# Kernel optimization log

Measured on AMD Instinct MI355X. Metric: run time of the kernel, lower is better.

## Reference

```python
import jax, jax.numpy as jnp
import numpy as np

BLANK = 0
T, N, C, S = 1024, 64, 128, 128


def setup_inputs() -> dict:
    key = jax.random.key(0)
    k1, k2, k3, k4 = jax.random.split(key, 4)
    logits = jax.random.normal(k1, (T, N, C), dtype=jnp.float32)
    log_probs = jax.nn.log_softmax(logits, axis=-1)
    targets = jax.random.randint(k2, (N, S), 1, C).astype(jnp.int64)  # non-blank labels
    input_lengths = jax.random.randint(k3, (N,), T // 2, T + 1).astype(jnp.int32)
    target_lengths = jax.random.randint(k4, (N,), S // 2, S + 1).astype(jnp.int32)
    return {"log_probs": log_probs, "targets": targets,
            "input_lengths": input_lengths, "target_lengths": target_lengths}


def _ctc_loss(log_probs, targets, input_lengths, target_lengths):
    Tt, Nn, Cc = log_probs.shape
    Ss = targets.shape[1]
    Sx = 2 * Ss + 1  # extended target length (blanks interleaved)
    neg_inf = jnp.asarray(-jnp.inf, log_probs.dtype)

    ext = jnp.full((Nn, Sx), BLANK, dtype=jnp.int32).at[:, 1::2].set(targets.astype(jnp.int32))
    # emission log-prob of each extended state at each time: [T, N, Sx]
    emit = jnp.take_along_axis(log_probs, jnp.broadcast_to(ext[None], (Tt, Nn, Sx)), axis=2)
    # skip transition allowed when label[s] != label[s-2] (and s >= 2)
    skip = jnp.concatenate([jnp.zeros((Nn, 2), bool), ext[:, 2:] != ext[:, :-2]], axis=1)

    # faithful to the torch code: alphas initialized to ZEROS, then states 0,1 set
    alpha0 = jnp.zeros((Nn, Sx), log_probs.dtype)
    alpha0 = alpha0.at[:, 0].set(emit[0, :, 0]).at[:, 1].set(emit[0, :, 1])

    pad1 = jnp.full((Nn, 1), neg_inf, log_probs.dtype)
    pad2 = jnp.full((Nn, 2), neg_inf, log_probs.dtype)

    def step(alpha, emit_t):
        a_m1 = jnp.concatenate([pad1, alpha[:, :-1]], axis=1)
        a_m2 = jnp.where(skip, jnp.concatenate([pad2, alpha[:, :-2]], axis=1), neg_inf)
        new = jax.nn.logsumexp(jnp.stack([alpha, a_m1, a_m2]), axis=0) + emit_t
        return new, new

    _, rest = jax.lax.scan(step, alpha0, emit[1:])
    alphas = jnp.concatenate([alpha0[None], rest], axis=0)  # [T, N, Sx]

    n_idx = jnp.arange(Nn)
    v = alphas[input_lengths - 1, n_idx, 2 * target_lengths - 1]  # [N]
    # original: loss = -logsumexp over batch, then .mean() of a scalar (identity)
    return -jax.nn.logsumexp(v)


def reference(log_probs, targets, input_lengths, target_lengths):
    return _ctc_loss(log_probs, targets, input_lengths, target_lengths)
```

## Files before the change

kernel.cpp:

```cpp
#include <hip/hip_runtime.h>
#include <math.h>

#define TT 1024
#define NN 64
#define CC 128
#define SS 128
#define CH 32
#define NCHUNK 32

typedef float f4 __attribute__((ext_vector_type(4)));

#define DPP_QP_XOR1   0xB1
#define DPP_QP_XOR2   0x4E
#define DPP_WAVE_SHR1 0x138
#define DPP_ROW_MIRR  0x140
#define DPP_HALF_MIRR 0x141
#define DPP_BCAST15   0x142
#define DPP_BCAST31   0x143

template <int CTRL>
__device__ __forceinline__ float dpp_max_stage(float v) {
    int p = __builtin_amdgcn_update_dpp(__float_as_int(v), __float_as_int(v),
                                        CTRL, 0xF, 0xF, false);
    return fmaxf(v, __int_as_float(p));
}
__device__ __forceinline__ float dpp_shr1(float v) {
    int p = __builtin_amdgcn_update_dpp(0, __float_as_int(v),
                                        DPP_WAVE_SHR1, 0xF, 0xF, true);
    return __int_as_float(p);
}

#define DSR(dst, addr, off) \
    asm volatile("ds_read_b128 %0, %1 offset:" #off : "=v"(dst) : "v"(addr))
#define LGKM(n) do { \
    asm volatile("s_waitcnt lgkmcnt(" #n ")" ::: "memory"); \
    __builtin_amdgcn_sched_barrier(0); } while (0)
#define ISSUE(mi, oea, oeb, opq) do { \
    DSR(gea[mi], base_e, oea); DSR(geb[mi], base_e, oeb); \
    DSR(gpq[mi], base_pq, opq); } while (0)

__global__ __launch_bounds__(320, 1) void ctc_scan(
    const float* __restrict__ lp,
    const int*   __restrict__ targets,
    const int*   __restrict__ ilen,
    const int*   __restrict__ tlen,
    float*       __restrict__ v_out)
{
    const int n    = blockIdx.x;
    const int tid  = threadIdx.x;
    const int wv   = tid >> 6;
    const int lane = tid & 63;

    __shared__ float4 s_e[2][CH / 2][64];
    __shared__ float4 s_pb4[2][CH / 4];

    const int tgA = targets[n * SS + 2 * lane];
    const int tgB = targets[n * SS + 2 * lane + 1];
    const float* lpn = lp + (size_t)n * CC;

    if (wv != 0) {
        const int w = wv - 1;
        float va[8], vc[8];
#pragma unroll
        for (int i = 0; i < 4; ++i) {
            const int k = w + 4 * i;
            const float* rowa = lpn + (size_t)(1 + 2 * k) * (NN * CC);
            const float* rowb = lpn + (size_t)(2 + 2 * k) * (NN * CC);
            va[2*i]   = rowa[tgA]; vc[2*i]   = rowa[tgB];
            va[2*i+1] = rowb[tgA]; vc[2*i+1] = rowb[tgB];
        }
        float pbv = 0.f;
        if (lane < 8) pbv = lpn[(size_t)(1 + w * 8 + lane) * (NN * CC)];
#pragma unroll
        for (int i = 0; i < 4; ++i) {
            const int k = w + 4 * i;
            s_e[0][k][lane] = make_float4(__expf(va[2*i]),   __expf(vc[2*i]),
                                          __expf(va[2*i+1]), __expf(vc[2*i+1]));
        }
        if (lane < 8) ((float*)s_pb4[0])[w * 8 + lane] = __expf(pbv);
    }

    const int tgBm = (lane > 0) ? targets[n * SS + 2 * lane - 1] : -1;
    const float k1f = (lane > 0 && tgA != tgBm) ? 1.f : 0.f;
    const float k3f = (tgB != tgA) ? 1.f : 0.f;
    const int il    = ilen[n];
    const int vs    = 2 * tlen[n] - 1;
    const int vlane = vs >> 2;

    float a0 = 1.f, a1 = 1.f, a2 = 1.f, a3 = 1.f, ls = 0.f;
    if (wv == 0) {
        a0 = (lane == 0) ? __expf(lpn[0])   : 1.f;
        a1 = (lane == 0) ? __expf(lpn[tgA]) : 1.f;
    }
    float a3p = (lane == 0) ? 0.f : 1.f;
    float mr = 1.f, inv = 1.f;

    const unsigned base_e0  = (unsigned)(size_t)(void*)&s_e[0][0][lane];
    const unsigned base_pq0 = (unsigned)(size_t)(void*)&s_pb4[0][0];

    __syncthreads();

    for (int cc = 0; cc < NCHUNK; ++cc) {
        const int b = cc & 1;
        if (wv == 0) {
            const int t0 = 1 + cc * CH;
            const bool cap = ((unsigned)(il - 1 - t0) < (unsigned)CH);
            const unsigned base_e  = base_e0  + (unsigned)(b << 14);
            const unsigned base_pq = base_pq0 + (unsigned)(b << 7);

            f4 gea[3], geb[3], gpq[3];

            auto group4 = [&](const f4& ea, const f4& eb, const f4& pq, int jbase) {
#pragma unroll
                for (int c = 0; c < 4; ++c) {
                    const int j = jbase + c;
                    const float cpa = (c==0)?ea[0]:(c==1)?ea[2]:(c==2)?eb[0]:eb[2];
                    const float cpc = (c==0)?ea[1]:(c==1)?ea[3]:(c==2)?eb[1]:eb[3];
                    const float cpb = pq[c];

                    float nb3 = fmaf(k3f, a1, a3 + a2) * cpc;
                    float a3pn = dpp_shr1(nb3);
                    float nb0 = (a0 + a3p) * cpb;
                    float nb1 = fmaf(k1f, a3p, a0 + a1) * cpa;
                    float nb2 = (a2 + a1) * cpb;

                    const int jj = j & 7;
                    if      (jj == 0) mr = fmaxf(fmaxf(nb0, nb1), fmaxf(nb2, nb3));
                    else if (jj == 1) mr = dpp_max_stage<DPP_QP_XOR1>(mr);
                    else if (jj == 2) mr = dpp_max_stage<DPP_QP_XOR2>(mr);
                    else if (jj == 3) mr = dpp_max_stage<DPP_HALF_MIRR>(mr);
                    else if (jj == 4) mr = dpp_max_stage<DPP_ROW_MIRR>(mr);
                    else if (jj == 5) mr = dpp_max_stage<DPP_BCAST15>(mr);
                    else if (jj == 6) mr = dpp_max_stage<DPP_BCAST31>(mr);
                    else {
                        const float mru = __int_as_float(
                            __builtin_amdgcn_readlane(__float_as_int(mr), 63));
                        inv = 1.0f / mru;
                        ls += __logf(mru);
                        nb0 *= inv; nb1 *= inv; nb2 *= inv; nb3 *= inv;
                    }

                    if (cap) {
                        const int t = t0 + j;
                        if (t == il - 1 && lane == vlane)
                            v_out[n] = __logf((vs & 2) ? nb3 : nb1) + ls;
                    }

                    a0 = nb0; a1 = nb1; a2 = nb2; a3 = nb3;
                    if (jj == 7) a3pn *= inv;
                    a3p = a3pn;
                }
            };

            ISSUE(0, 0,     1024,  0);
            ISSUE(1, 2048,  3072,  16);
            ISSUE(2, 4096,  5120,  32);  LGKM(6); group4(gea[0], geb[0], gpq[0], 0);
            ISSUE(0, 6144,  7168,  48);  LGKM(6); group4(gea[1], geb[1], gpq[1], 4);
            ISSUE(1, 8192,  9216,  64);  LGKM(6); group4(gea[2], geb[2], gpq[2], 8);
            ISSUE(2, 10240, 11264, 80);  LGKM(6); group4(gea[0], geb[0], gpq[0], 12);
            ISSUE(0, 12288, 13312, 96);  LGKM(6); group4(gea[1], geb[1], gpq[1], 16);
            ISSUE(1, 14336, 15360, 112); LGKM(6); group4(gea[2], geb[2], gpq[2], 20);
                                         LGKM(3); group4(gea[0], geb[0], gpq[0], 24);
                                         LGKM(0); group4(gea[1], geb[1], gpq[1], 28);
        } else if (cc + 1 < NCHUNK) {
            const int w  = wv - 1;
            const int b2 = (cc + 1) & 1;
            const int t0 = 1 + (cc + 1) * CH;
            float va[8], vc[8];
#pragma unroll
            for (int i = 0; i < 4; ++i) {
                const int k = w + 4 * i;
                int ta = t0 + 2 * k;     if (ta > TT - 1) ta = TT - 1;
                int tb = t0 + 2 * k + 1; if (tb > TT - 1) tb = TT - 1;
                const float* rowa = lpn + (size_t)ta * (NN * CC);
                const float* rowb = lpn + (size_t)tb * (NN * CC);
                va[2*i]   = rowa[tgA]; vc[2*i]   = rowa[tgB];
                va[2*i+1] = rowb[tgA]; vc[2*i+1] = rowb[tgB];
            }
            float pbv = 0.f;
            if (lane < 8) {
                int tp = t0 + w * 8 + lane; if (tp > TT - 1) tp = TT - 1;
                pbv = lpn[(size_t)tp * (NN * CC)];
            }
#pragma unroll
            for (int i = 0; i < 4; ++i) {
                const int k = w + 4 * i;
                s_e[b2][k][lane] = make_float4(__expf(va[2*i]),   __expf(vc[2*i]),
                                               __expf(va[2*i+1]), __expf(vc[2*i+1]));
            }
            if (lane < 8) ((float*)s_pb4[b2])[w * 8 + lane] = __expf(pbv);
        }
        __syncthreads();
    }
}

__global__ void ctc_reduce(const float* __restrict__ v, float* __restrict__ out)
{
    const int lane = threadIdx.x;
    float x = v[lane];
    float m = x;
#pragma unroll
    for (int off = 32; off > 0; off >>= 1) m = fmaxf(m, __shfl_xor(m, off));
    float e = __expf(x - m);
#pragma unroll
    for (int off = 32; off > 0; off >>= 1) e += __shfl_xor(e, off);
    if (lane == 0) out[0] = -(m + __logf(e));
}

extern "C" void kernel_launch(void* const* d_in, const int* in_sizes, int n_in,
                              void* d_out, int out_size, void* d_ws, size_t ws_size,
                              hipStream_t stream) {
    const float* lp      = (const float*)d_in[0];
    const int*   targets = (const int*)d_in[1];
    const int*   ilen    = (const int*)d_in[2];
    const int*   tlen    = (const int*)d_in[3];

    float* v   = (float*)d_ws;
    float* out = (float*)d_out;

    ctc_scan<<<NN, 320, 0, stream>>>(lp, targets, ilen, tlen, v);
    ctc_reduce<<<1, 64, 0, stream>>>(v, out);
}
```

Before: 73.73 us.

## Stage full log-prob rows into LDS via async global_load_lds, prefetch two chunks ahead

The producer waves no longer gather scattered per-label elements from global memory. They now copy whole contiguous 128-float time rows into a double-buffered LDS staging area with global_load_lds, issued two chunks ahead, and then gather and exponentiate from LDS. The aim is coalesced, asynchronous loads with deeper prefetch, hiding global latency behind the serial scan wave. The __syncthreads is replaced by a raw s_barrier with manual vmcnt/lgkmcnt waits, which adds risk around buffer reuse and ordering.

```diff
diff --git a/kernel.cpp b/kernel.cpp
--- a/kernel.cpp
+++ b/kernel.cpp
@@ -7,6 +7,7 @@
 #define SS 128
 #define CH 32
 #define NCHUNK 32
+#define NC (NN * CC)
 
 typedef float f4 __attribute__((ext_vector_type(4)));
 
@@ -35,9 +36,13 @@
 #define LGKM(n) do { \
     asm volatile("s_waitcnt lgkmcnt(" #n ")" ::: "memory"); \
     __builtin_amdgcn_sched_barrier(0); } while (0)
+#define VMC(n) do { \
+    asm volatile("s_waitcnt vmcnt(" #n ")" ::: "memory"); \
+    __builtin_amdgcn_sched_barrier(0); } while (0)
 #define ISSUE(mi, oea, oeb, opq) do { \
     DSR(gea[mi], base_e, oea); DSR(geb[mi], base_e, oeb); \
     DSR(gpq[mi], base_pq, opq); } while (0)
+#define BARRIER() asm volatile("s_barrier" ::: "memory")
 
 __global__ __launch_bounds__(320, 1) void ctc_scan(
     const float* __restrict__ lp,
@@ -51,6 +56,7 @@
     const int wv   = tid >> 6;
     const int lane = tid & 63;
 
+    __shared__ float  s_rows[2][CH][CC];
     __shared__ float4 s_e[2][CH / 2][64];
     __shared__ float4 s_pb4[2][CH / 4];
 
@@ -58,26 +64,42 @@
     const int tgB = targets[n * SS + 2 * lane + 1];
     const float* lpn = lp + (size_t)n * CC;
 
+    const int w  = wv - 1;
+    const int r0 = w * 8;
+
+    auto issue_rows = [&](int c, int buf) {
+#pragma unroll
+        for (int i = 0; i < 4; ++i) {
+            const int r = r0 + 2 * i;
+            int t = 1 + c * CH + r + (lane >> 5);
+            if (t > TT - 1) t = TT - 1;
+            const float* src = lpn + (size_t)t * NC + (lane & 31) * 4;
+            __builtin_amdgcn_global_load_lds(
+                (const __attribute__((address_space(1))) void*)src,
+                (__attribute__((address_space(3))) void*)&s_rows[buf][r][0],
+                16, 0, 0);
+        }
+    };
+    auto gather = [&](int buf, int ebuf) {
+#pragma unroll
+        for (int i = 0; i < 4; ++i) {
+            const int rA = r0 + 2 * i, rB = rA + 1;
+            const float pa0 = s_rows[buf][rA][tgA], pc0 = s_rows[buf][rA][tgB];
+            const float pa1 = s_rows[buf][rB][tgA], pc1 = s_rows[buf][rB][tgB];
+            s_e[ebuf][(r0 >> 1) + i][lane] =
+                make_float4(__expf(pa0), __expf(pc0), __expf(pa1), __expf(pc1));
+        }
+        if (lane < 8) {
+            const float pbv = s_rows[buf][r0 + lane][0];
+            ((float*)s_pb4[ebuf])[r0 + lane] = __expf(pbv);
+        }
+    };
+
     if (wv != 0) {
-        const int w = wv - 1;
-        float va[8], vc[8];
-#pragma unroll
-        for (int i = 0; i < 4; ++i) {
-            const int k = w + 4 * i;
-            const float* rowa = lpn + (size_t)(1 + 2 * k) * (NN * CC);
-            const float* rowb = lpn + (size_t)(2 + 2 * k) * (NN * CC);
-            va[2*i]   = rowa[tgA]; vc[2*i]   = rowa[tgB];
-            va[2*i+1] = rowb[tgA]; vc[2*i+1] = rowb[tgB];
-        }
-        float pbv = 0.f;
-        if (lane < 8) pbv = lpn[(size_t)(1 + w * 8 + lane) * (NN * CC)];
-#pragma unroll
-        for (int i = 0; i < 4; ++i) {
-            const int k = w + 4 * i;
-            s_e[0][k][lane] = make_float4(__expf(va[2*i]),   __expf(vc[2*i]),
-                                          __expf(va[2*i+1]), __expf(vc[2*i+1]));
-        }
-        if (lane < 8) ((float*)s_pb4[0])[w * 8 + lane] = __expf(pbv);
+        issue_rows(0, 0);
+        issue_rows(1, 1);
+        VMC(4);
+        gather(0, 0);
     }
 
     const int tgBm = (lane > 0) ? targets[n * SS + 2 * lane - 1] : -1;
@@ -162,35 +184,13 @@
             ISSUE(1, 14336, 15360, 112); LGKM(6); group4(gea[2], geb[2], gpq[2], 20);
                                          LGKM(3); group4(gea[0], geb[0], gpq[0], 24);
                                          LGKM(0); group4(gea[1], geb[1], gpq[1], 28);
-        } else if (cc + 1 < NCHUNK) {
-            const int w  = wv - 1;
-            const int b2 = (cc + 1) & 1;
-            const int t0 = 1 + (cc + 1) * CH;
-            float va[8], vc[8];
-#pragma unroll
-            for (int i = 0; i < 4; ++i) {
-                const int k = w + 4 * i;
-                int ta = t0 + 2 * k;     if (ta > TT - 1) ta = TT - 1;
-                int tb = t0 + 2 * k + 1; if (tb > TT - 1) tb = TT - 1;
-                const float* rowa = lpn + (size_t)ta * (NN * CC);
-                const float* rowb = lpn + (size_t)tb * (NN * CC);
-                va[2*i]   = rowa[tgA]; vc[2*i]   = rowa[tgB];
-                va[2*i+1] = rowb[tgA]; vc[2*i+1] = rowb[tgB];
-            }
-            float pbv = 0.f;
-            if (lane < 8) {
-                int tp = t0 + w * 8 + lane; if (tp > TT - 1) tp = TT - 1;
-                pbv = lpn[(size_t)tp * (NN * CC)];
-            }
-#pragma unroll
-            for (int i = 0; i < 4; ++i) {
-                const int k = w + 4 * i;
-                s_e[b2][k][lane] = make_float4(__expf(va[2*i]),   __expf(vc[2*i]),
-                                               __expf(va[2*i+1]), __expf(vc[2*i+1]));
-            }
-            if (lane < 8) ((float*)s_pb4[b2])[w * 8 + lane] = __expf(pbv);
-        }
-        __syncthreads();
+        } else {
+            issue_rows(cc + 2, cc & 1);
+            VMC(4);
+            if (cc + 1 < NCHUNK) gather((cc + 1) & 1, (cc + 1) & 1);
+            asm volatile("s_waitcnt lgkmcnt(0)" ::: "memory");
+        }
+        BARRIER();
     }
 }
 
```

New measurement: 71.63 us (median of 2 runs). 2.9% less time.
